# Performance work log

Hardware: AMD Instinct MI355X
Metric: run time of the kernel (lower is better)

## Reference

```python
import jax, jax.numpy as jnp
import numpy as np


def setup_inputs() -> dict:
    key = jax.random.key(0)
    k1, k2, k3, k4 = jax.random.split(key, 4)
    B, C, H, Wd = 32, 512, 32, 32
    sparse_dim, dict_size, feature_dim = 1024, 1024, 512
    x = jax.random.normal(k1, (B, C, H, Wd), dtype=jnp.float32)
    dictionary = jax.random.normal(k2, (dict_size, feature_dim), dtype=jnp.float32)
    # scale W, S like the LISTA init (|| . || ~ O(1)) so iterates stay bounded
    W = jax.random.normal(k3, (sparse_dim, feature_dim), dtype=jnp.float32) * 0.02
    S = jax.random.normal(k4, (sparse_dim, sparse_dim), dtype=jnp.float32) * 0.02
    thresh = jnp.float32(0.1)
    return {"x": x, "dictionary": dictionary, "W": W, "S": S, "thresh": thresh, "num_steps": 5}


def _soft_threshold(z, thresh):
    return jnp.sign(z) * jnp.maximum(jnp.abs(z) - thresh, 0.0)


def reference(x, dictionary, W, S, thresh, num_steps):
    B, C, H, Wd = x.shape
    sparse_dim = S.shape[0]
    # [B,C,H,W] -> [B*H*W, C]
    x_flat = jnp.transpose(x, (0, 2, 3, 1)).reshape(-1, C)
    dict_norm = dictionary / jnp.linalg.norm(dictionary, axis=1, keepdims=True)
    # W @ x^T is loop-invariant; compute once. [K, N]
    Wx = W @ x_flat.T
    z = jnp.zeros((sparse_dim, x_flat.shape[0]), dtype=x.dtype)
    for _ in range(num_steps):
        z = z + Wx
        z = z - S @ z
        z = _soft_threshold(z, thresh)
    # [K,N] -> [B,K,H,W]
    z = jnp.transpose(z.T.reshape(B, H, Wd, sparse_dim), (0, 3, 1, 2))
    return (z, dict_norm)
```

## Files before the change

### kernel.cpp

```cpp
#include <hip/hip_runtime.h>
#include <hip/hip_bf16.h>

typedef __bf16 bf16_t;
typedef __bf16 bf16x4 __attribute__((ext_vector_type(4)));
typedef __bf16 bf16x8 __attribute__((ext_vector_type(8)));
typedef float f32x4 __attribute__((ext_vector_type(4)));

#define GLOAD_LDS16(g, l)                                                      \
  __builtin_amdgcn_global_load_lds(                                            \
      (const __attribute__((address_space(1))) void*)(g),                      \
      (__attribute__((address_space(3))) void*)(l), 16, 0, 0)

#define MFMA(a, b, c) __builtin_amdgcn_mfma_f32_16x16x32_bf16((a), (b), (c), 0, 0, 0)

__global__ __launch_bounds__(512, 2) void gemm_kernel(
    const bf16_t* __restrict__ A, const bf16_t* __restrict__ Bt,
    int Kd, int Nc, int mode,
    const bf16_t* __restrict__ WxIn, bf16_t* __restrict__ UnextOrWx,
    float* __restrict__ Out, const float* __restrict__ thresh_p)
{
  __shared__ __align__(16) char smem[147456];
  bf16_t* lds = (bf16_t*)smem;

  const int tid = threadIdx.x;
  const int wid = tid >> 6, lane = tid & 63;
  const int wr = wid >> 1, wc = wid & 1;
  const int lr = lane & 15, kg = lane >> 4;

  const int per = gridDim.x >> 3;
  const int logical = (blockIdx.x & 7) * per + (blockIdx.x >> 3);
  const int ntn = Nc >> 7;
  const int tileN = (logical % ntn) << 7;
  const int tileM = (logical / ntn) << 8;
  const int NT = Kd >> 6;

  size_t offA[4]; int dstA[4];
  #pragma unroll
  for (int j = 0; j < 4; ++j) {
    const int f = j * 512 + tid;
    const int row = f >> 3, u = f & 7;
    const int ug = u ^ (row & 7);
    offA[j] = (size_t)(tileM + row) * Kd + ug * 8;
    dstA[j] = f * 8;
  }
  size_t offB[2]; int dstB[2];
  #pragma unroll
  for (int j = 0; j < 2; ++j) {
    const int f = j * 512 + tid;
    const int col = f >> 3, u = f & 7;
    const int ug = u ^ (col & 7);
    offB[j] = (size_t)(tileN + col) * Kd + ug * 8;
    dstB[j] = 16384 + f * 8;
  }

  auto readA = [&](int mi, int ks, int bs) -> bf16x8 {
    const int R = wr * 64 + mi * 16 + lr;
    const int ul = (ks * 4 + kg) ^ (R & 7);
    return *(const bf16x8*)(lds + bs + R * 64 + ul * 8);
  };
  auto readB = [&](int ni, int ks, int bs) -> bf16x8 {
    const int C = wc * 64 + ni * 16 + lr;
    const int ul = (ks * 4 + kg) ^ (C & 7);
    return *(const bf16x8*)(lds + bs + 16384 + C * 64 + ul * 8);
  };

  f32x4 acc[4][4] = {};
  bf16x8 a0[4], b0[4], a1[4], b1[4];

  #pragma unroll
  for (int j = 0; j < 4; ++j) GLOAD_LDS16(A + offA[j], lds + dstA[j]);
  #pragma unroll
  for (int j = 0; j < 2; ++j) GLOAD_LDS16(Bt + offB[j], lds + dstB[j]);
  if (NT > 1) {
    #pragma unroll
    for (int j = 0; j < 4; ++j) GLOAD_LDS16(A + offA[j] + 64, lds + 24576 + dstA[j]);
    #pragma unroll
    for (int j = 0; j < 2; ++j) GLOAD_LDS16(Bt + offB[j] + 64, lds + 24576 + dstB[j]);
  }
  asm volatile("s_waitcnt vmcnt(6)" ::: "memory");
  __builtin_amdgcn_s_barrier();

  int buf = 0, sb3 = 2;
  for (int t = 0; t < NT; ++t) {
    const int bs = buf * 24576;
    const int sbs = sb3 * 24576;
    const int ts = (t + 2 < NT) ? t + 2 : t + 2 - NT;
    const size_t ko = (size_t)ts << 6;

    GLOAD_LDS16(A + offA[0] + ko, lds + sbs + dstA[0]);
    GLOAD_LDS16(A + offA[1] + ko, lds + sbs + dstA[1]);
    GLOAD_LDS16(A + offA[2] + ko, lds + sbs + dstA[2]);
    GLOAD_LDS16(A + offA[3] + ko, lds + sbs + dstA[3]);
    GLOAD_LDS16(Bt + offB[0] + ko, lds + sbs + dstB[0]);
    GLOAD_LDS16(Bt + offB[1] + ko, lds + sbs + dstB[1]);

    #pragma unroll
    for (int mi = 0; mi < 4; ++mi) a0[mi] = readA(mi, 0, bs);
    #pragma unroll
    for (int ni = 0; ni < 4; ++ni) b0[ni] = readB(ni, 0, bs);
    #pragma unroll
    for (int mi = 0; mi < 4; ++mi) a1[mi] = readA(mi, 1, bs);
    #pragma unroll
    for (int ni = 0; ni < 4; ++ni) b1[ni] = readB(ni, 1, bs);

    #pragma unroll
    for (int mi = 0; mi < 4; ++mi)
      #pragma unroll
      for (int ni = 0; ni < 4; ++ni)
        acc[mi][ni] = MFMA(a0[mi], b0[ni], acc[mi][ni]);
    #pragma unroll
    for (int mi = 0; mi < 4; ++mi)
      #pragma unroll
      for (int ni = 0; ni < 4; ++ni)
        acc[mi][ni] = MFMA(a1[mi], b1[ni], acc[mi][ni]);

    asm volatile("s_waitcnt vmcnt(6)" ::: "memory");
    __builtin_amdgcn_s_barrier();

    buf = (buf == 2) ? 0 : buf + 1;
    sb3 = (sb3 == 2) ? 0 : sb3 + 1;
  }

  const float th = *thresh_p;

  if (mode <= 1) {
    asm volatile("s_waitcnt vmcnt(0)" ::: "memory");
    __syncthreads();
    float* Tl = (float*)smem;
    #pragma unroll
    for (int c = 0; c < 8; ++c) {
      if (c) __syncthreads();
      if (wr == (c >> 1)) {
        #pragma unroll
        for (int mj = 0; mj < 2; ++mj) {
          const int mi = (c & 1) * 2 + mj;
          const int rl = mj * 16 + kg * 4;
          #pragma unroll
          for (int ni = 0; ni < 4; ++ni) {
            const int cl = wc * 64 + ni * 16 + lr;
            #pragma unroll
            for (int r = 0; r < 4; ++r)
              Tl[(rl + r) * 132 + cl] = acc[mi][ni][r];
          }
        }
      }
      __syncthreads();
      #pragma unroll
      for (int j = 0; j < 2; ++j) {
        const int f  = j * 512 + tid;
        const int rl = f >> 5;
        const int c4 = (f & 31) * 4;
        const f32x4 v = *(const f32x4*)&Tl[rl * 132 + c4];
        const int grow = tileM + c * 32 + rl;
        const size_t gidx = (size_t)grow * Nc + tileN + c4;
        bf16x4 ov;
        if (mode == 1) {
          const bf16x4 wx = *(const bf16x4*)&WxIn[gidx];
          #pragma unroll
          for (int e = 0; e < 4; ++e) {
            const float a  = fabsf(v[e]) - th;
            const float zn = (a > 0.f) ? copysignf(a, v[e]) : 0.f;
            ov[e] = (bf16_t)(zn + (float)wx[e]);
          }
        } else {
          #pragma unroll
          for (int e = 0; e < 4; ++e) ov[e] = (bf16_t)v[e];
        }
        *(bf16x4*)&UnextOrWx[gidx] = ov;
      }
    }
  } else {
    #pragma unroll
    for (int mi = 0; mi < 4; ++mi)
      #pragma unroll
      for (int ni = 0; ni < 4; ++ni)
        #pragma unroll
        for (int r = 0; r < 4; ++r) {
          const float v = acc[mi][ni][r];
          const float a = fabsf(v) - th;
          acc[mi][ni][r] = (a > 0.f) ? copysignf(a, v) : 0.f;
        }
    asm volatile("s_waitcnt vmcnt(0)" ::: "memory");
    __syncthreads();
    float* Tl = (float*)smem;
    const int    bb    = tileM >> 10;
    const size_t obase = (size_t)bb * 1048576 + (size_t)(tileM & 1023);
    #pragma unroll
    for (int ch = 0; ch < 4; ++ch) {
      if (ch) __syncthreads();
      if (wc == (ch >> 1)) {
        #pragma unroll
        for (int nj = 0; nj < 2; ++nj) {
          const int ni = (ch & 1) * 2 + nj;
          const int cp = nj * 16 + lr;
          #pragma unroll
          for (int mi = 0; mi < 4; ++mi)
            #pragma unroll
            for (int r = 0; r < 4; ++r)
              Tl[cp * 260 + wr * 64 + mi * 16 + kg * 4 + r] = acc[mi][ni][r];
        }
      }
      __syncthreads();
      #pragma unroll
      for (int j = 0; j < 4; ++j) {
        const int f  = j * 512 + tid;
        const int cp = f >> 6;
        const int p4 = (f & 63) * 4;
        const f32x4 v = *(const f32x4*)&Tl[cp * 260 + p4];
        *(f32x4*)&Out[obase + (size_t)(tileN + ch * 32 + cp) * 1024 + p4] = v;
      }
    }
  }
}

__global__ void make_T_castW_kernel(const float* __restrict__ S,
                                    bf16_t* __restrict__ T,
                                    const float* __restrict__ W,
                                    bf16_t* __restrict__ Wb) {
  const int idx = blockIdx.x * blockDim.x + threadIdx.x;
  const int i = idx >> 10, j = idx & 1023;
  T[idx] = (bf16_t)(((i == j) ? 1.0f : 0.0f) - S[idx]);
  if (idx < 524288) Wb[idx] = (bf16_t)W[idx];
}

__global__ void transpose_cast_x_kernel(const float* __restrict__ x,
                                        bf16_t* __restrict__ xt) {
  __shared__ float t[32][33];
  const int b  = blockIdx.z;
  const int p0 = blockIdx.x * 32;
  const int c0 = blockIdx.y * 32;
  const int tx = threadIdx.x, ty = threadIdx.y;
  #pragma unroll
  for (int i = 0; i < 32; i += 8)
    t[ty + i][tx] = x[((size_t)b * 512 + c0 + ty + i) * 1024 + p0 + tx];
  __syncthreads();
  #pragma unroll
  for (int i = 0; i < 32; i += 8)
    xt[((size_t)b * 1024 + p0 + ty + i) * 512 + c0 + tx] = (bf16_t)t[tx][ty + i];
}

__global__ void transpose_cast_w_kernel(const float* __restrict__ W,
                                        bf16_t* __restrict__ Wt) {
  __shared__ float t[32][33];
  const int j0 = blockIdx.x * 32;
  const int c0 = blockIdx.y * 32;
  const int tx = threadIdx.x, ty = threadIdx.y;
  #pragma unroll
  for (int i = 0; i < 32; i += 8)
    t[ty + i][tx] = W[(size_t)(j0 + ty + i) * 512 + c0 + tx];
  __syncthreads();
  #pragma unroll
  for (int i = 0; i < 32; i += 8)
    Wt[(size_t)(c0 + ty + i) * 1024 + j0 + tx] = (bf16_t)t[tx][ty + i];
}

__global__ void dict_norm_kernel(const float* __restrict__ dict,
                                 float* __restrict__ out) {
  const int row = blockIdx.x;
  const int tid = threadIdx.x;
  const float* r = dict + (size_t)row * 512;
  float s = 0.f;
  for (int i = tid; i < 512; i += 256) { float v = r[i]; s += v * v; }
  #pragma unroll
  for (int off = 32; off > 0; off >>= 1) s += __shfl_down(s, off);
  __shared__ float ps[4];
  if ((tid & 63) == 0) ps[tid >> 6] = s;
  __syncthreads();
  const float inv = 1.0f / sqrtf(ps[0] + ps[1] + ps[2] + ps[3]);
  for (int i = tid; i < 512; i += 256) out[(size_t)row * 512 + i] = r[i] * inv;
}

extern "C" void kernel_launch(void* const* d_in, const int* in_sizes, int n_in,
                              void* d_out, int out_size, void* d_ws, size_t ws_size,
                              hipStream_t stream) {
  const float* x      = (const float*)d_in[0];
  const float* dict   = (const float*)d_in[1];
  const float* W      = (const float*)d_in[2];
  const float* S      = (const float*)d_in[3];
  const float* thresh = (const float*)d_in[4];

  float* out = (float*)d_out;

  char* ws = (char*)d_ws;
  bf16_t* uA   = (bf16_t*)ws;
  bf16_t* uB   = (bf16_t*)(ws + 67108864);
  bf16_t* WxBf = (bf16_t*)(ws + 134217728);
  bf16_t* xt   = (bf16_t*)(ws + 201326592);
  bf16_t* Wbf  = (bf16_t*)(ws + 234881024);
  bf16_t* Tbf  = (bf16_t*)(ws + 235929600);

  bf16_t* WtBf = (bf16_t*)out;
  bf16_t* TWbf = WtBf + 524288;
  float* dnorm = out + 33554432;

  make_T_castW_kernel<<<dim3(2048), dim3(512), 0, stream>>>(S, Tbf, W, Wbf);
  transpose_cast_x_kernel<<<dim3(32, 16, 32), dim3(32, 8), 0, stream>>>(x, xt);
  transpose_cast_w_kernel<<<dim3(32, 16), dim3(32, 8), 0, stream>>>(W, WtBf);
  dict_norm_kernel<<<dim3(1024), dim3(256), 0, stream>>>(dict, dnorm);

  gemm_kernel<<<dim3(16), dim3(512), 0, stream>>>(
      Tbf, WtBf, 1024, 512, 0, nullptr, TWbf, nullptr, thresh);

  gemm_kernel<<<dim3(1024), dim3(512), 0, stream>>>(
      xt, Wbf, 512, 1024, 0, nullptr, WxBf, nullptr, thresh);

  gemm_kernel<<<dim3(1024), dim3(512), 0, stream>>>(
      xt, TWbf, 512, 1024, 1, WxBf, uA, nullptr, thresh);

  bf16_t* uc = uA; bf16_t* un = uB;
  for (int s = 0; s < 3; ++s) {
    gemm_kernel<<<dim3(1024), dim3(512), 0, stream>>>(
        uc, Tbf, 1024, 1024, 1, WxBf, un, nullptr, thresh);
    bf16_t* tmp = uc; uc = un; un = tmp;
  }
  gemm_kernel<<<dim3(1024), dim3(512), 0, stream>>>(
      uc, Tbf, 1024, 1024, 2, nullptr, nullptr, out, thresh);
}
```

Before: 542.1 us.

## Fuse Wx and first iteration GEMMs into dual-output kernel sharing A tiles

Replaces two separate GEMM launches that both read xt (one for Wx = x·W, one for x·(T·W) plus threshold) with a single kernel that stages one A tile and two B tiles per k-step and accumulates both products. The Wx result is written out and also added in-register to the thresholded second product, so xt is read once and WxBf does not have to be reread. In exchange it doubles the accumulator registers (two 4x4 f32x4 sets) and adds extra LDS round-trips in the epilogue, which may lower occupancy.

```diff
diff --git a/kernel.cpp b/kernel.cpp
--- a/kernel.cpp
+++ b/kernel.cpp
@@ -213,6 +213,172 @@
   }
 }
 
+__global__ __launch_bounds__(512, 2) void gemm_dual_kernel(
+    const bf16_t* __restrict__ A, const bf16_t* __restrict__ B1,
+    const bf16_t* __restrict__ B2,
+    bf16_t* __restrict__ WxOut, bf16_t* __restrict__ UOut,
+    const float* __restrict__ thresh_p)
+{
+  __shared__ __align__(16) char smem[131072];
+  bf16_t* lds = (bf16_t*)smem;
+
+  const int tid = threadIdx.x;
+  const int wid = tid >> 6, lane = tid & 63;
+  const int wr = wid >> 1, wc = wid & 1;
+  const int lr = lane & 15, kg = lane >> 4;
+
+  const int per = gridDim.x >> 3;
+  const int logical = (blockIdx.x & 7) * per + (blockIdx.x >> 3);
+  const int tileN = (logical & 7) << 7;
+  const int tileM = (logical >> 3) << 8;
+
+  size_t offA[4]; int dstA[4];
+  #pragma unroll
+  for (int j = 0; j < 4; ++j) {
+    const int f = j * 512 + tid;
+    const int row = f >> 3, u = f & 7;
+    const int ug = u ^ (row & 7);
+    offA[j] = (size_t)(tileM + row) * 512 + ug * 8;
+    dstA[j] = f * 8;
+  }
+  size_t offB[2]; int dstB1[2], dstB2[2];
+  #pragma unroll
+  for (int j = 0; j < 2; ++j) {
+    const int f = j * 512 + tid;
+    const int col = f >> 3, u = f & 7;
+    const int ug = u ^ (col & 7);
+    offB[j] = (size_t)(tileN + col) * 512 + ug * 8;
+    dstB1[j] = 16384 + f * 8;
+    dstB2[j] = 24576 + f * 8;
+  }
+
+  auto readA = [&](int mi, int ks, int bs) -> bf16x8 {
+    const int R = wr * 64 + mi * 16 + lr;
+    const int ul = (ks * 4 + kg) ^ (R & 7);
+    return *(const bf16x8*)(lds + bs + R * 64 + ul * 8);
+  };
+  auto readB = [&](int boff, int ni, int ks, int bs) -> bf16x8 {
+    const int C = wc * 64 + ni * 16 + lr;
+    const int ul = (ks * 4 + kg) ^ (C & 7);
+    return *(const bf16x8*)(lds + bs + boff + C * 64 + ul * 8);
+  };
+
+  f32x4 accW[4][4] = {}, accT[4][4] = {};
+  bf16x8 af[4], bw[4], bt[4];
+
+  auto stageTile = [&](int ts, int sbs) {
+    const size_t ko = (size_t)ts << 6;
+    #pragma unroll
+    for (int j = 0; j < 4; ++j) GLOAD_LDS16(A + offA[j] + ko, lds + sbs + dstA[j]);
+    #pragma unroll
+    for (int j = 0; j < 2; ++j) GLOAD_LDS16(B1 + offB[j] + ko, lds + sbs + dstB1[j]);
+    #pragma unroll
+    for (int j = 0; j < 2; ++j) GLOAD_LDS16(B2 + offB[j] + ko, lds + sbs + dstB2[j]);
+  };
+
+  stageTile(0, 0);
+  asm volatile("s_waitcnt vmcnt(0)" ::: "memory");
+  __builtin_amdgcn_s_barrier();
+
+  for (int t = 0; t < 8; ++t) {
+    const int bs  = (t & 1) << 15;
+    const int sbs = bs ^ 32768;
+    stageTile((t + 1 < 8) ? t + 1 : 0, sbs);
+
+    #pragma unroll
+    for (int ks = 0; ks < 2; ++ks) {
+      #pragma unroll
+      for (int mi = 0; mi < 4; ++mi) af[mi] = readA(mi, ks, bs);
+      #pragma unroll
+      for (int ni = 0; ni < 4; ++ni) bw[ni] = readB(16384, ni, ks, bs);
+      #pragma unroll
+      for (int ni = 0; ni < 4; ++ni) bt[ni] = readB(24576, ni, ks, bs);
+      #pragma unroll
+      for (int mi = 0; mi < 4; ++mi)
+        #pragma unroll
+        for (int ni = 0; ni < 4; ++ni) {
+          accW[mi][ni] = MFMA(af[mi], bw[ni], accW[mi][ni]);
+          accT[mi][ni] = MFMA(af[mi], bt[ni], accT[mi][ni]);
+        }
+    }
+
+    asm volatile("s_waitcnt vmcnt(0)" ::: "memory");
+    __builtin_amdgcn_s_barrier();
+  }
+
+  const float th = *thresh_p;
+  asm volatile("s_waitcnt vmcnt(0)" ::: "memory");
+  __syncthreads();
+  float* Tl = (float*)smem;
+
+  #pragma unroll
+  for (int c = 0; c < 8; ++c) {
+    if (c) __syncthreads();
+    if (wr == (c >> 1)) {
+      #pragma unroll
+      for (int mj = 0; mj < 2; ++mj) {
+        const int mi = (c & 1) * 2 + mj;
+        const int rl = mj * 16 + kg * 4;
+        #pragma unroll
+        for (int ni = 0; ni < 4; ++ni) {
+          const int cl = wc * 64 + ni * 16 + lr;
+          #pragma unroll
+          for (int r = 0; r < 4; ++r)
+            Tl[(rl + r) * 132 + cl] = accW[mi][ni][r];
+        }
+      }
+    }
+    __syncthreads();
+    f32x4 vw[2];
+    #pragma unroll
+    for (int j = 0; j < 2; ++j) {
+      const int f  = j * 512 + tid;
+      const int rl = f >> 5;
+      const int c4 = (f & 31) * 4;
+      vw[j] = *(const f32x4*)&Tl[rl * 132 + c4];
+      const int grow = tileM + c * 32 + rl;
+      const size_t gidx = (size_t)grow * 1024 + tileN + c4;
+      bf16x4 ov;
+      #pragma unroll
+      for (int e = 0; e < 4; ++e) ov[e] = (bf16_t)vw[j][e];
+      *(bf16x4*)&WxOut[gidx] = ov;
+    }
+    __syncthreads();
+    if (wr == (c >> 1)) {
+      #pragma unroll
+      for (int mj = 0; mj < 2; ++mj) {
+        const int mi = (c & 1) * 2 + mj;
+        const int rl = mj * 16 + kg * 4;
+        #pragma unroll
+        for (int ni = 0; ni < 4; ++ni) {
+          const int cl = wc * 64 + ni * 16 + lr;
+          #pragma unroll
+          for (int r = 0; r < 4; ++r)
+            Tl[(rl + r) * 132 + cl] = accT[mi][ni][r];
+        }
+      }
+    }
+    __syncthreads();
+    #pragma unroll
+    for (int j = 0; j < 2; ++j) {
+      const int f  = j * 512 + tid;
+      const int rl = f >> 5;
+      const int c4 = (f & 31) * 4;
+      const f32x4 vt = *(const f32x4*)&Tl[rl * 132 + c4];
+      const int grow = tileM + c * 32 + rl;
+      const size_t gidx = (size_t)grow * 1024 + tileN + c4;
+      bf16x4 ov;
+      #pragma unroll
+      for (int e = 0; e < 4; ++e) {
+        const float a  = fabsf(vt[e]) - th;
+        const float zn = (a > 0.f) ? copysignf(a, vt[e]) : 0.f;
+        ov[e] = (bf16_t)(zn + vw[j][e]);
+      }
+      *(bf16x4*)&UOut[gidx] = ov;
+    }
+  }
+}
+
 __global__ void make_T_castW_kernel(const float* __restrict__ S,
                                     bf16_t* __restrict__ T,
                                     const float* __restrict__ W,
@@ -301,11 +467,8 @@
   gemm_kernel<<<dim3(16), dim3(512), 0, stream>>>(
       Tbf, WtBf, 1024, 512, 0, nullptr, TWbf, nullptr, thresh);
 
-  gemm_kernel<<<dim3(1024), dim3(512), 0, stream>>>(
-      xt, Wbf, 512, 1024, 0, nullptr, WxBf, nullptr, thresh);
-
-  gemm_kernel<<<dim3(1024), dim3(512), 0, stream>>>(
-      xt, TWbf, 512, 1024, 1, WxBf, uA, nullptr, thresh);
+  gemm_dual_kernel<<<dim3(1024), dim3(512), 0, stream>>>(
+      xt, Wbf, TWbf, WxBf, uA, thresh);
 
   bf16_t* uc = uA; bf16_t* un = uB;
   for (int s = 0; s < 3; ++s) {
```

Result: faster. 511.7 us (-5.6%).
